# Performance work log

Measured on AMD Instinct MI355X. Metric: run time of the kernel, lower is better.

## Reference

```python
import jax, jax.numpy as jnp
import numpy as np

B, F, CHUNK = 4096, 1024, 128  # batch, features, scan chunk size
EPS = 1e-5  # nn.LayerNorm default eps


def setup_inputs() -> dict:
    key = jax.random.key(0)
    k1, k2 = jax.random.split(key, 2)
    x = jax.random.normal(k1, (B, F), dtype=jnp.float32)
    W = jax.random.normal(k2, (F, F), dtype=jnp.float32) * 0.5  # init_weight = randn*0.5
    b = jnp.zeros((F,), dtype=jnp.float32)
    gamma = jnp.ones((F,), dtype=jnp.float32)   # LayerNorm weight
    beta = jnp.zeros((F,), dtype=jnp.float32)   # LayerNorm bias
    return {"x": x, "W": W, "b": b, "gamma": gamma, "beta": beta}


def reference(x, W, b, gamma, beta):
    # LayerNorm over last dim (biased variance, as torch)
    mu = jnp.mean(x, axis=-1, keepdims=True)
    var = jnp.mean(jnp.square(x - mu), axis=-1, keepdims=True)
    xn = (x - mu) * jax.lax.rsqrt(var + EPS) * gamma + beta  # [B, F]

    # Tropical max-plus matmul: out[b, i] = max_k xn[b, k] + W[k, i]
    # Chunk the batch to avoid materializing the full [B, F, F] broadcast-add.
    xc = xn.reshape(B // CHUNK, CHUNK, F)

    def step(_, xb):  # xb: [CHUNK, F]
        o = jnp.max(xb[:, :, None] + W[None, :, :], axis=1)  # [CHUNK, F]
        return None, o

    _, out = jax.lax.scan(step, None, xc)
    out = out.reshape(B, F)

    # Tropical bias: elementwise max with learned threshold b
    return jnp.maximum(out, b)
```

## Files before the change

### kernel.cpp

```cpp
#include <hip/hip_runtime.h>
#include <math.h>

#define F 1024
#define BM 128
#define BN 128
#define BK 16

typedef _Float16 h2 __attribute__((ext_vector_type(2)));
typedef _Float16 h4 __attribute__((ext_vector_type(4)));
typedef _Float16 h8 __attribute__((ext_vector_type(8)));
typedef float v4f __attribute__((ext_vector_type(4)));

#define SHUF2(v, i, j) __builtin_shufflevector(v, v, i, j)
#define SHUF4(v, a, b, c, d) __builtin_shufflevector(v, v, a, b, c, d)

static __device__ __forceinline__ h2 pk_add_blo(h2 a, h2 b) {
  h2 d;
  asm("v_pk_add_f16 %0, %1, %2 op_sel:[0,0] op_sel_hi:[0,1]"
      : "=v"(d) : "v"(a), "v"(b));
  return d;
}
static __device__ __forceinline__ h2 pk_add_bhi(h2 a, h2 b) {
  h2 d;
  asm("v_pk_add_f16 %0, %1, %2 op_sel:[1,0] op_sel_hi:[1,1]"
      : "=v"(d) : "v"(a), "v"(b));
  return d;
}
static __device__ __forceinline__ h2 pk_max(h2 a, h2 b) {
  h2 d;
  asm("v_pk_max_f16 %0, %1, %2" : "=v"(d) : "v"(a), "v"(b));
  return d;
}

__global__ __launch_bounds__(256) void ln_cvt_kernel(const float* __restrict__ x,
                                                     const float* __restrict__ gamma,
                                                     const float* __restrict__ beta,
                                                     const float* __restrict__ Wm,
                                                     _Float16* __restrict__ xnh,
                                                     _Float16* __restrict__ Wh) {
  const int lane = threadIdx.x & 63;
  const int wv = threadIdx.x >> 6;
  const int row = blockIdx.x * 4 + wv;
  const float4* xr = (const float4*)(x + (size_t)row * F);
  float4 v[4];
  float s = 0.f;
#pragma unroll
  for (int j = 0; j < 4; ++j) {
    v[j] = xr[lane + 64 * j];
    s += v[j].x + v[j].y + v[j].z + v[j].w;
  }
#pragma unroll
  for (int off = 32; off; off >>= 1) s += __shfl_xor(s, off, 64);
  const float mu = s * (1.0f / F);
  float sq = 0.f;
#pragma unroll
  for (int j = 0; j < 4; ++j) {
    v[j].x -= mu; v[j].y -= mu; v[j].z -= mu; v[j].w -= mu;
    sq += v[j].x * v[j].x + v[j].y * v[j].y + v[j].z * v[j].z + v[j].w * v[j].w;
  }
#pragma unroll
  for (int off = 32; off; off >>= 1) sq += __shfl_xor(sq, off, 64);
  const float r = rsqrtf(sq * (1.0f / F) + 1e-5f);
  const float4* g4 = (const float4*)gamma;
  const float4* b4 = (const float4*)beta;
  h4* o = (h4*)(xnh + (size_t)row * F);
#pragma unroll
  for (int j = 0; j < 4; ++j) {
    const int idx = lane + 64 * j;
    const float4 g = g4[idx];
    const float4 bb = b4[idx];
    h4 ov = {(_Float16)(v[j].x * r * g.x + bb.x),
             (_Float16)(v[j].y * r * g.y + bb.y),
             (_Float16)(v[j].z * r * g.z + bb.z),
             (_Float16)(v[j].w * r * g.w + bb.w)};
    o[idx] = ov;
  }
  {
    const int i = (int)blockIdx.x * 256 + threadIdx.x;
    const v4f wv4 = ((const v4f*)Wm)[i];
    h4 wo = {(_Float16)wv4.x, (_Float16)wv4.y, (_Float16)wv4.z, (_Float16)wv4.w};
    ((h4*)Wh)[i] = wo;
  }
}

__global__ __launch_bounds__(256) void trop_h(const _Float16* __restrict__ A,
                                              const _Float16* __restrict__ Wh,
                                              const float* __restrict__ bias,
                                              _Float16* __restrict__ dsth,
                                              float* __restrict__ outf,
                                              int ntiles, int totrows, int fuse) {
  __shared__ _Float16 As[2][BM][BK + 4];
  __shared__ _Float16 Bs[2][BK][BN];

  const int tid = threadIdx.x;
  const int tx = tid & 15;
  const int ty = tid >> 4;
  const int row0 = blockIdx.y * BM;
  const int col0 = blockIdx.x * BN;
  const int kbase = blockIdx.z * ntiles * BK;

  const int am2 = tid >> 1, aj = tid & 1;
  const int bi = tid >> 4, bj = tid & 15;

  const _Float16* Asrc = A + (size_t)(row0 + am2) * F + kbase + aj * 8;
  const _Float16* Bsrc = Wh + (size_t)(kbase + bi) * F + col0 + bj * 8;

  const _Float16 NEG = (_Float16)(-60000.0f);
  h2 acc[8][4];
#pragma unroll
  for (int m = 0; m < 8; ++m)
#pragma unroll
    for (int np = 0; np < 4; ++np) acc[m][np] = (h2){NEG, NEG};

  {
    h8 a_st = *(const h8*)Asrc;
    h8 b_st = *(const h8*)Bsrc;
    *(h4*)&As[0][am2][aj * 8] = SHUF4(a_st, 0, 1, 2, 3);
    *(h4*)&As[0][am2][aj * 8 + 4] = SHUF4(a_st, 4, 5, 6, 7);
    *(h8*)&Bs[0][bi][bj * 8] = b_st;
  }
  __syncthreads();

  for (int kt = 0; kt < ntiles; ++kt) {
    const int cur = kt & 1;
    h8 a_st, b_st;
    if (kt + 1 < ntiles) {
      a_st = *(const h8*)(Asrc + (kt + 1) * BK);
      b_st = *(const h8*)(Bsrc + (size_t)(kt + 1) * BK * F);
    }

#pragma unroll
    for (int kq = 0; kq < 4; ++kq) {
      h4 a4[8];
#pragma unroll
      for (int m = 0; m < 8; ++m) a4[m] = *(const h4*)&As[cur][ty * 8 + m][kq * 4];
#pragma unroll
      for (int kp = 0; kp < 2; ++kp) {
        const int k = kq * 4 + kp * 2;
        const h8 bA = *(const h8*)&Bs[cur][k][tx * 8];
        const h8 bB = *(const h8*)&Bs[cur][k + 1][tx * 8];
        h2 b0[4], b1[4];
        b0[0] = SHUF2(bA, 0, 1); b0[1] = SHUF2(bA, 2, 3);
        b0[2] = SHUF2(bA, 4, 5); b0[3] = SHUF2(bA, 6, 7);
        b1[0] = SHUF2(bB, 0, 1); b1[1] = SHUF2(bB, 2, 3);
        b1[2] = SHUF2(bB, 4, 5); b1[3] = SHUF2(bB, 6, 7);
#pragma unroll
        for (int m = 0; m < 8; ++m) {
          const h2 a = kp ? SHUF2(a4[m], 2, 3) : SHUF2(a4[m], 0, 1);
#pragma unroll
          for (int np = 0; np < 4; ++np) {
            const h2 s0 = pk_add_blo(a, b0[np]);
            const h2 s1 = pk_add_bhi(a, b1[np]);
            acc[m][np] = pk_max(acc[m][np], pk_max(s0, s1));
          }
        }
      }
    }

    if (kt + 1 < ntiles) {
      const int nxt = cur ^ 1;
      *(h4*)&As[nxt][am2][aj * 8] = SHUF4(a_st, 0, 1, 2, 3);
      *(h4*)&As[nxt][am2][aj * 8 + 4] = SHUF4(a_st, 4, 5, 6, 7);
      *(h8*)&Bs[nxt][bi][bj * 8] = b_st;
      __syncthreads();
    }
  }

  if (fuse) {
    const float4 bv0 = *(const float4*)(bias + col0 + tx * 8);
    const float4 bv1 = *(const float4*)(bias + col0 + tx * 8 + 4);
#pragma unroll
    for (int m = 0; m < 8; ++m) {
      float* orow = outf + (size_t)(row0 + ty * 8 + m) * F + col0 + tx * 8;
      float4 o0, o1;
      o0.x = fmaxf((float)acc[m][0].x, bv0.x);
      o0.y = fmaxf((float)acc[m][0].y, bv0.y);
      o0.z = fmaxf((float)acc[m][1].x, bv0.z);
      o0.w = fmaxf((float)acc[m][1].y, bv0.w);
      o1.x = fmaxf((float)acc[m][2].x, bv1.x);
      o1.y = fmaxf((float)acc[m][2].y, bv1.y);
      o1.z = fmaxf((float)acc[m][3].x, bv1.z);
      o1.w = fmaxf((float)acc[m][3].y, bv1.w);
      *(float4*)orow = o0;
      *(float4*)(orow + 4) = o1;
    }
  } else {
    _Float16* base = dsth + (size_t)blockIdx.z * totrows * F;
#pragma unroll
    for (int m = 0; m < 8; ++m) {
      h8 ov = {acc[m][0].x, acc[m][0].y, acc[m][1].x, acc[m][1].y,
               acc[m][2].x, acc[m][2].y, acc[m][3].x, acc[m][3].y};
      *(h8*)(base + (size_t)(row0 + ty * 8 + m) * F + col0 + tx * 8) = ov;
    }
  }
}

template <int NP>
__global__ __launch_bounds__(256) void combineNh(const _Float16* __restrict__ p,
                                                 size_t plane,
                                                 const float* __restrict__ bias,
                                                 float* __restrict__ out) {
  const int i = blockIdx.x * 256 + threadIdx.x;
  h8 v = ((const h8*)p)[i];
  h2* vv = (h2*)&v;
#pragma unroll
  for (int q = 1; q < NP; ++q) {
    const h8 u = ((const h8*)(p + (size_t)q * plane))[i];
    const h2* uu = (const h2*)&u;
#pragma unroll
    for (int j = 0; j < 4; ++j) vv[j] = pk_max(vv[j], uu[j]);
  }
  const int nb = (i & (F / 8 - 1)) * 8;
  const v4f bb0 = *(const v4f*)(bias + nb);
  const v4f bb1 = *(const v4f*)(bias + nb + 4);
  float4* o4 = (float4*)(out + (size_t)i * 8);
  float4 o0, o1;
  o0.x = fmaxf((float)v[0], bb0.x);
  o0.y = fmaxf((float)v[1], bb0.y);
  o0.z = fmaxf((float)v[2], bb0.z);
  o0.w = fmaxf((float)v[3], bb0.w);
  o1.x = fmaxf((float)v[4], bb1.x);
  o1.y = fmaxf((float)v[5], bb1.y);
  o1.z = fmaxf((float)v[6], bb1.z);
  o1.w = fmaxf((float)v[7], bb1.w);
  o4[0] = o0;
  o4[1] = o1;
}

extern "C" void kernel_launch(void* const* d_in, const int* in_sizes, int n_in,
                              void* d_out, int out_size, void* d_ws, size_t ws_size,
                              hipStream_t stream) {
  const float* x = (const float*)d_in[0];
  const float* Wm = (const float*)d_in[1];
  const float* bias = (const float*)d_in[2];
  const float* gamma = (const float*)d_in[3];
  const float* beta = (const float*)d_in[4];
  float* out = (float*)d_out;

  const int Brows = in_sizes[0] / F;
  const size_t plane = (size_t)Brows * F;

  _Float16* xnh = (_Float16*)d_ws;
  _Float16* Wh = xnh + plane;
  _Float16* parts = Wh + (size_t)F * F;

  ln_cvt_kernel<<<Brows / 4, 256, 0, stream>>>(x, gamma, beta, Wm, xnh, Wh);

  const size_t need4 = (5 * plane + (size_t)F * F) * sizeof(_Float16);
  const size_t need1 = (plane + (size_t)F * F) * sizeof(_Float16);
  if (ws_size >= need4) {
    dim3 grid(F / BN, Brows / BM, 4);
    trop_h<<<grid, 256, 0, stream>>>(xnh, Wh, bias, parts, nullptr,
                                     (F / BK) / 4, Brows, 0);
    combineNh<4><<<(int)(plane / 2048), 256, 0, stream>>>(parts, plane, bias, out);
  } else if (ws_size >= need1) {
    dim3 grid(F / BN, Brows / BM, 1);
    trop_h<<<grid, 256, 0, stream>>>(xnh, Wh, bias, nullptr, out, F / BK, Brows, 1);
  }
}
```

Before: 220.1 us.

## Switch tropical matmul from packed fp16 to fp32 with max3

Replaces the packed-fp16 max-plus inner loop with an fp32 version using v_max3_f32 over two k-steps, reading W directly in fp32 and storing A transposed (K-major) in shared memory. The LayerNorm kernel now writes fp32 and no longer converts W to fp16. This improves numerical accuracy and removes a conversion pass, but doubles shared/global traffic per element and loses the 2-wide packed math throughput.

```diff
diff --git a/kernel.cpp b/kernel.cpp
--- a/kernel.cpp
+++ b/kernel.cpp
@@ -11,19 +11,9 @@
 typedef _Float16 h8 __attribute__((ext_vector_type(8)));
 typedef float v4f __attribute__((ext_vector_type(4)));
 
-#define SHUF2(v, i, j) __builtin_shufflevector(v, v, i, j)
-#define SHUF4(v, a, b, c, d) __builtin_shufflevector(v, v, a, b, c, d)
-
-static __device__ __forceinline__ h2 pk_add_blo(h2 a, h2 b) {
-  h2 d;
-  asm("v_pk_add_f16 %0, %1, %2 op_sel:[0,0] op_sel_hi:[0,1]"
-      : "=v"(d) : "v"(a), "v"(b));
-  return d;
-}
-static __device__ __forceinline__ h2 pk_add_bhi(h2 a, h2 b) {
-  h2 d;
-  asm("v_pk_add_f16 %0, %1, %2 op_sel:[1,0] op_sel_hi:[1,1]"
-      : "=v"(d) : "v"(a), "v"(b));
+static __device__ __forceinline__ float fmax3(float a, float b, float c) {
+  float d;
+  asm("v_max3_f32 %0, %1, %2, %3" : "=v"(d) : "v"(a), "v"(b), "v"(c));
   return d;
 }
 static __device__ __forceinline__ h2 pk_max(h2 a, h2 b) {
@@ -32,12 +22,10 @@
   return d;
 }
 
-__global__ __launch_bounds__(256) void ln_cvt_kernel(const float* __restrict__ x,
-                                                     const float* __restrict__ gamma,
-                                                     const float* __restrict__ beta,
-                                                     const float* __restrict__ Wm,
-                                                     _Float16* __restrict__ xnh,
-                                                     _Float16* __restrict__ Wh) {
+__global__ __launch_bounds__(256) void ln_kernel(const float* __restrict__ x,
+                                                 const float* __restrict__ gamma,
+                                                 const float* __restrict__ beta,
+                                                 float* __restrict__ xn) {
   const int lane = threadIdx.x & 63;
   const int wv = threadIdx.x >> 6;
   const int row = blockIdx.x * 4 + wv;
@@ -63,34 +51,29 @@
   const float r = rsqrtf(sq * (1.0f / F) + 1e-5f);
   const float4* g4 = (const float4*)gamma;
   const float4* b4 = (const float4*)beta;
-  h4* o = (h4*)(xnh + (size_t)row * F);
+  float4* o = (float4*)(xn + (size_t)row * F);
 #pragma unroll
   for (int j = 0; j < 4; ++j) {
     const int idx = lane + 64 * j;
     const float4 g = g4[idx];
     const float4 bb = b4[idx];
-    h4 ov = {(_Float16)(v[j].x * r * g.x + bb.x),
-             (_Float16)(v[j].y * r * g.y + bb.y),
-             (_Float16)(v[j].z * r * g.z + bb.z),
-             (_Float16)(v[j].w * r * g.w + bb.w)};
+    float4 ov;
+    ov.x = v[j].x * r * g.x + bb.x;
+    ov.y = v[j].y * r * g.y + bb.y;
+    ov.z = v[j].z * r * g.z + bb.z;
+    ov.w = v[j].w * r * g.w + bb.w;
     o[idx] = ov;
   }
-  {
-    const int i = (int)blockIdx.x * 256 + threadIdx.x;
-    const v4f wv4 = ((const v4f*)Wm)[i];
-    h4 wo = {(_Float16)wv4.x, (_Float16)wv4.y, (_Float16)wv4.z, (_Float16)wv4.w};
-    ((h4*)Wh)[i] = wo;
-  }
-}
-
-__global__ __launch_bounds__(256) void trop_h(const _Float16* __restrict__ A,
-                                              const _Float16* __restrict__ Wh,
-                                              const float* __restrict__ bias,
-                                              _Float16* __restrict__ dsth,
-                                              float* __restrict__ outf,
-                                              int ntiles, int totrows, int fuse) {
-  __shared__ _Float16 As[2][BM][BK + 4];
-  __shared__ _Float16 Bs[2][BK][BN];
+}
+
+__global__ __launch_bounds__(256, 4) void trop_f(const float* __restrict__ A,
+                                                 const float* __restrict__ Wm,
+                                                 const float* __restrict__ bias,
+                                                 _Float16* __restrict__ dsth,
+                                                 float* __restrict__ outf,
+                                                 int ntiles, int totrows, int fuse) {
+  __shared__ float As[2][BK][BM + 4];
+  __shared__ float Bs[2][BK][BN];
 
   const int tid = threadIdx.x;
   const int tx = tid & 15;
@@ -99,98 +82,119 @@
   const int col0 = blockIdx.x * BN;
   const int kbase = blockIdx.z * ntiles * BK;
 
-  const int am2 = tid >> 1, aj = tid & 1;
-  const int bi = tid >> 4, bj = tid & 15;
-
-  const _Float16* Asrc = A + (size_t)(row0 + am2) * F + kbase + aj * 8;
-  const _Float16* Bsrc = Wh + (size_t)(kbase + bi) * F + col0 + bj * 8;
-
-  const _Float16 NEG = (_Float16)(-60000.0f);
-  h2 acc[8][4];
+  const int am = tid >> 2;
+  const int ak = (tid & 3) << 2;
+  const int bk = tid >> 5;
+  const int bn = (tid & 31) << 2;
+
+  const float* Arow0 = A + (size_t)(row0 + am) * F + kbase + ak;
+  const float* Arow1 = A + (size_t)(row0 + am + 64) * F + kbase + ak;
+  const float* Wrow0 = Wm + (size_t)(kbase + bk) * F + col0 + bn;
+  const float* Wrow1 = Wm + (size_t)(kbase + bk + 8) * F + col0 + bn;
+
+  float acc[8][8];
 #pragma unroll
   for (int m = 0; m < 8; ++m)
 #pragma unroll
-    for (int np = 0; np < 4; ++np) acc[m][np] = (h2){NEG, NEG};
+    for (int n = 0; n < 8; ++n) acc[m][n] = -INFINITY;
 
   {
-    h8 a_st = *(const h8*)Asrc;
-    h8 b_st = *(const h8*)Bsrc;
-    *(h4*)&As[0][am2][aj * 8] = SHUF4(a_st, 0, 1, 2, 3);
-    *(h4*)&As[0][am2][aj * 8 + 4] = SHUF4(a_st, 4, 5, 6, 7);
-    *(h8*)&Bs[0][bi][bj * 8] = b_st;
+    const float4 a0s = *(const float4*)(Arow0);
+    const float4 a1s = *(const float4*)(Arow1);
+    const float4 b0s = *(const float4*)(Wrow0);
+    const float4 b1s = *(const float4*)(Wrow1);
+    As[0][ak + 0][am] = a0s.x;
+    As[0][ak + 1][am] = a0s.y;
+    As[0][ak + 2][am] = a0s.z;
+    As[0][ak + 3][am] = a0s.w;
+    As[0][ak + 0][am + 64] = a1s.x;
+    As[0][ak + 1][am + 64] = a1s.y;
+    As[0][ak + 2][am + 64] = a1s.z;
+    As[0][ak + 3][am + 64] = a1s.w;
+    *(float4*)&Bs[0][bk][bn] = b0s;
+    *(float4*)&Bs[0][bk + 8][bn] = b1s;
   }
   __syncthreads();
 
   for (int kt = 0; kt < ntiles; ++kt) {
     const int cur = kt & 1;
-    h8 a_st, b_st;
+    float4 a0s, a1s, b0s, b1s;
     if (kt + 1 < ntiles) {
-      a_st = *(const h8*)(Asrc + (kt + 1) * BK);
-      b_st = *(const h8*)(Bsrc + (size_t)(kt + 1) * BK * F);
-    }
-
-#pragma unroll
-    for (int kq = 0; kq < 4; ++kq) {
-      h4 a4[8];
-#pragma unroll
-      for (int m = 0; m < 8; ++m) a4[m] = *(const h4*)&As[cur][ty * 8 + m][kq * 4];
-#pragma unroll
-      for (int kp = 0; kp < 2; ++kp) {
-        const int k = kq * 4 + kp * 2;
-        const h8 bA = *(const h8*)&Bs[cur][k][tx * 8];
-        const h8 bB = *(const h8*)&Bs[cur][k + 1][tx * 8];
-        h2 b0[4], b1[4];
-        b0[0] = SHUF2(bA, 0, 1); b0[1] = SHUF2(bA, 2, 3);
-        b0[2] = SHUF2(bA, 4, 5); b0[3] = SHUF2(bA, 6, 7);
-        b1[0] = SHUF2(bB, 0, 1); b1[1] = SHUF2(bB, 2, 3);
-        b1[2] = SHUF2(bB, 4, 5); b1[3] = SHUF2(bB, 6, 7);
-#pragma unroll
-        for (int m = 0; m < 8; ++m) {
-          const h2 a = kp ? SHUF2(a4[m], 2, 3) : SHUF2(a4[m], 0, 1);
-#pragma unroll
-          for (int np = 0; np < 4; ++np) {
-            const h2 s0 = pk_add_blo(a, b0[np]);
-            const h2 s1 = pk_add_bhi(a, b1[np]);
-            acc[m][np] = pk_max(acc[m][np], pk_max(s0, s1));
+      const int k0 = (kt + 1) * BK;
+      a0s = *(const float4*)(Arow0 + k0);
+      a1s = *(const float4*)(Arow1 + k0);
+      b0s = *(const float4*)(Wrow0 + (size_t)k0 * F);
+      b1s = *(const float4*)(Wrow1 + (size_t)k0 * F);
+    }
+
+#pragma unroll
+    for (int k = 0; k < BK; k += 2) {
+      float a0[8], a1[8];
+      *(float4*)&a0[0] = *(const float4*)&As[cur][k][ty * 8];
+      *(float4*)&a0[4] = *(const float4*)&As[cur][k][ty * 8 + 4];
+      *(float4*)&a1[0] = *(const float4*)&As[cur][k + 1][ty * 8];
+      *(float4*)&a1[4] = *(const float4*)&As[cur][k + 1][ty * 8 + 4];
+#pragma unroll
+      for (int h = 0; h < 2; ++h) {
+        float b0[4], b1[4];
+        *(float4*)&b0[0] = *(const float4*)&Bs[cur][k][h * 64 + tx * 4];
+        *(float4*)&b1[0] = *(const float4*)&Bs[cur][k + 1][h * 64 + tx * 4];
+#pragma unroll
+        for (int m = 0; m < 8; ++m)
+#pragma unroll
+          for (int n = 0; n < 4; ++n) {
+            const float t0 = a0[m] + b0[n];
+            const float t1 = a1[m] + b1[n];
+            acc[m][h * 4 + n] = fmax3(acc[m][h * 4 + n], t0, t1);
           }
-        }
       }
     }
 
     if (kt + 1 < ntiles) {
       const int nxt = cur ^ 1;
-      *(h4*)&As[nxt][am2][aj * 8] = SHUF4(a_st, 0, 1, 2, 3);
-      *(h4*)&As[nxt][am2][aj * 8 + 4] = SHUF4(a_st, 4, 5, 6, 7);
-      *(h8*)&Bs[nxt][bi][bj * 8] = b_st;
+      As[nxt][ak + 0][am] = a0s.x;
+      As[nxt][ak + 1][am] = a0s.y;
+      As[nxt][ak + 2][am] = a0s.z;
+      As[nxt][ak + 3][am] = a0s.w;
+      As[nxt][ak + 0][am + 64] = a1s.x;
+      As[nxt][ak + 1][am + 64] = a1s.y;
+      As[nxt][ak + 2][am + 64] = a1s.z;
+      As[nxt][ak + 3][am + 64] = a1s.w;
+      *(float4*)&Bs[nxt][bk][bn] = b0s;
+      *(float4*)&Bs[nxt][bk + 8][bn] = b1s;
       __syncthreads();
     }
   }
 
   if (fuse) {
-    const float4 bv0 = *(const float4*)(bias + col0 + tx * 8);
-    const float4 bv1 = *(const float4*)(bias + col0 + tx * 8 + 4);
+    const float4 bv0 = *(const float4*)(bias + col0 + tx * 4);
+    const float4 bv1 = *(const float4*)(bias + col0 + 64 + tx * 4);
 #pragma unroll
     for (int m = 0; m < 8; ++m) {
-      float* orow = outf + (size_t)(row0 + ty * 8 + m) * F + col0 + tx * 8;
+      float* orow = outf + (size_t)(row0 + ty * 8 + m) * F + col0 + tx * 4;
       float4 o0, o1;
-      o0.x = fmaxf((float)acc[m][0].x, bv0.x);
-      o0.y = fmaxf((float)acc[m][0].y, bv0.y);
-      o0.z = fmaxf((float)acc[m][1].x, bv0.z);
-      o0.w = fmaxf((float)acc[m][1].y, bv0.w);
-      o1.x = fmaxf((float)acc[m][2].x, bv1.x);
-      o1.y = fmaxf((float)acc[m][2].y, bv1.y);
-      o1.z = fmaxf((float)acc[m][3].x, bv1.z);
-      o1.w = fmaxf((float)acc[m][3].y, bv1.w);
+      o0.x = fmaxf(acc[m][0], bv0.x);
+      o0.y = fmaxf(acc[m][1], bv0.y);
+      o0.z = fmaxf(acc[m][2], bv0.z);
+      o0.w = fmaxf(acc[m][3], bv0.w);
+      o1.x = fmaxf(acc[m][4], bv1.x);
+      o1.y = fmaxf(acc[m][5], bv1.y);
+      o1.z = fmaxf(acc[m][6], bv1.z);
+      o1.w = fmaxf(acc[m][7], bv1.w);
       *(float4*)orow = o0;
-      *(float4*)(orow + 4) = o1;
+      *(float4*)(orow + 64) = o1;
     }
   } else {
     _Float16* base = dsth + (size_t)blockIdx.z * totrows * F;
 #pragma unroll
     for (int m = 0; m < 8; ++m) {
-      h8 ov = {acc[m][0].x, acc[m][0].y, acc[m][1].x, acc[m][1].y,
-               acc[m][2].x, acc[m][2].y, acc[m][3].x, acc[m][3].y};
-      *(h8*)(base + (size_t)(row0 + ty * 8 + m) * F + col0 + tx * 8) = ov;
+      _Float16* orow = base + (size_t)(row0 + ty * 8 + m) * F + col0 + tx * 4;
+      h4 o0 = {(_Float16)acc[m][0], (_Float16)acc[m][1],
+               (_Float16)acc[m][2], (_Float16)acc[m][3]};
+      h4 o1 = {(_Float16)acc[m][4], (_Float16)acc[m][5],
+               (_Float16)acc[m][6], (_Float16)acc[m][7]};
+      *(h4*)orow = o0;
+      *(h4*)(orow + 64) = o1;
     }
   }
 }
@@ -240,21 +244,20 @@
   const int Brows = in_sizes[0] / F;
   const size_t plane = (size_t)Brows * F;
 
-  _Float16* xnh = (_Float16*)d_ws;
-  _Float16* Wh = xnh + plane;
-  _Float16* parts = Wh + (size_t)F * F;
-
-  ln_cvt_kernel<<<Brows / 4, 256, 0, stream>>>(x, gamma, beta, Wm, xnh, Wh);
-
-  const size_t need4 = (5 * plane + (size_t)F * F) * sizeof(_Float16);
-  const size_t need1 = (plane + (size_t)F * F) * sizeof(_Float16);
+  float* xn = (float*)d_ws;
+  _Float16* parts = (_Float16*)(xn + plane);
+
+  ln_kernel<<<Brows / 4, 256, 0, stream>>>(x, gamma, beta, xn);
+
+  const size_t need4 = plane * sizeof(float) + 4 * plane * sizeof(_Float16);
+  const size_t need1 = plane * sizeof(float);
   if (ws_size >= need4) {
     dim3 grid(F / BN, Brows / BM, 4);
-    trop_h<<<grid, 256, 0, stream>>>(xnh, Wh, bias, parts, nullptr,
+    trop_f<<<grid, 256, 0, stream>>>(xn, Wm, bias, parts, nullptr,
                                      (F / BK) / 4, Brows, 0);
     combineNh<4><<<(int)(plane / 2048), 256, 0, stream>>>(parts, plane, bias, out);
   } else if (ws_size >= need1) {
     dim3 grid(F / BN, Brows / BM, 1);
-    trop_h<<<grid, 256, 0, stream>>>(xnh, Wh, bias, nullptr, out, F / BK, Brows, 1);
-  }
-}
+    trop_f<<<grid, 256, 0, stream>>>(xn, Wm, bias, nullptr, out, F / BK, Brows, 1);
+  }
+}
```

New measurement: 210.3 us. 1.05x faster.

## Accumulate max-plus in fp32 via fma_mix and max3 with transposed A tile

Applied to the files above, without the earlier changes.

Replaces the packed fp16 add/max inner loop with v_fma_mix_f32, which adds fp16 inputs into fp32 results, and v_max3_f32, which folds two k-steps per max. Accumulators become fp32 (64 floats per thread). The A tile is stored k-major in shared memory so rows can be read as vectors, and the B column mapping becomes interleaved (tx*4 and 64+tx*4) to change the LDS access pattern. This gives more accurate accumulation. The cost is roughly twice as many VALU ops per output, since the packed fp16 ops did two elements each, plus higher register pressure under a 4-waves launch bound.

```diff
diff --git a/kernel.cpp b/kernel.cpp
--- a/kernel.cpp
+++ b/kernel.cpp
@@ -12,18 +12,34 @@
 typedef float v4f __attribute__((ext_vector_type(4)));
 
 #define SHUF2(v, i, j) __builtin_shufflevector(v, v, i, j)
-#define SHUF4(v, a, b, c, d) __builtin_shufflevector(v, v, a, b, c, d)
-
-static __device__ __forceinline__ h2 pk_add_blo(h2 a, h2 b) {
-  h2 d;
-  asm("v_pk_add_f16 %0, %1, %2 op_sel:[0,0] op_sel_hi:[0,1]"
-      : "=v"(d) : "v"(a), "v"(b));
-  return d;
-}
-static __device__ __forceinline__ h2 pk_add_bhi(h2 a, h2 b) {
-  h2 d;
-  asm("v_pk_add_f16 %0, %1, %2 op_sel:[1,0] op_sel_hi:[1,1]"
-      : "=v"(d) : "v"(a), "v"(b));
+
+static __device__ __forceinline__ float mix_ll(h2 a, h2 b) {
+  float d;
+  asm("v_fma_mix_f32 %0, %1, 1.0, %2 op_sel:[0,0,0] op_sel_hi:[1,0,1]"
+      : "=v"(d) : "v"(a), "v"(b));
+  return d;
+}
+static __device__ __forceinline__ float mix_lh(h2 a, h2 b) {
+  float d;
+  asm("v_fma_mix_f32 %0, %1, 1.0, %2 op_sel:[0,0,1] op_sel_hi:[1,0,1]"
+      : "=v"(d) : "v"(a), "v"(b));
+  return d;
+}
+static __device__ __forceinline__ float mix_hl(h2 a, h2 b) {
+  float d;
+  asm("v_fma_mix_f32 %0, %1, 1.0, %2 op_sel:[1,0,0] op_sel_hi:[1,0,1]"
+      : "=v"(d) : "v"(a), "v"(b));
+  return d;
+}
+static __device__ __forceinline__ float mix_hh(h2 a, h2 b) {
+  float d;
+  asm("v_fma_mix_f32 %0, %1, 1.0, %2 op_sel:[1,0,1] op_sel_hi:[1,0,1]"
+      : "=v"(d) : "v"(a), "v"(b));
+  return d;
+}
+static __device__ __forceinline__ float fmax3(float a, float b, float c) {
+  float d;
+  asm("v_max3_f32 %0, %1, %2, %3" : "=v"(d) : "v"(a), "v"(b), "v"(c));
   return d;
 }
 static __device__ __forceinline__ h2 pk_max(h2 a, h2 b) {
@@ -83,13 +99,13 @@
   }
 }
 
-__global__ __launch_bounds__(256) void trop_h(const _Float16* __restrict__ A,
-                                              const _Float16* __restrict__ Wh,
-                                              const float* __restrict__ bias,
-                                              _Float16* __restrict__ dsth,
-                                              float* __restrict__ outf,
-                                              int ntiles, int totrows, int fuse) {
-  __shared__ _Float16 As[2][BM][BK + 4];
+__global__ __launch_bounds__(256, 4) void trop_m(const _Float16* __restrict__ A,
+                                                 const _Float16* __restrict__ Wh,
+                                                 const float* __restrict__ bias,
+                                                 _Float16* __restrict__ dsth,
+                                                 float* __restrict__ outf,
+                                                 int ntiles, int totrows, int fuse) {
+  __shared__ _Float16 As[2][BK][BM + 8];
   __shared__ _Float16 Bs[2][BK][BN];
 
   const int tid = threadIdx.x;
@@ -99,25 +115,26 @@
   const int col0 = blockIdx.x * BN;
   const int kbase = blockIdx.z * ntiles * BK;
 
-  const int am2 = tid >> 1, aj = tid & 1;
-  const int bi = tid >> 4, bj = tid & 15;
-
-  const _Float16* Asrc = A + (size_t)(row0 + am2) * F + kbase + aj * 8;
-  const _Float16* Bsrc = Wh + (size_t)(kbase + bi) * F + col0 + bj * 8;
-
-  const _Float16 NEG = (_Float16)(-60000.0f);
-  h2 acc[8][4];
+  const int ar = tid >> 1;
+  const int akj = (tid & 1) * 8;
+  const int bkr = tid >> 4;
+  const int bcg = (tid & 15) * 8;
+
+  const _Float16* Asrc = A + (size_t)(row0 + ar) * F + kbase + akj;
+  const _Float16* Bsrc = Wh + (size_t)(kbase + bkr) * F + col0 + bcg;
+
+  float acc[8][8];
 #pragma unroll
   for (int m = 0; m < 8; ++m)
 #pragma unroll
-    for (int np = 0; np < 4; ++np) acc[m][np] = (h2){NEG, NEG};
+    for (int n = 0; n < 8; ++n) acc[m][n] = -INFINITY;
 
   {
-    h8 a_st = *(const h8*)Asrc;
-    h8 b_st = *(const h8*)Bsrc;
-    *(h4*)&As[0][am2][aj * 8] = SHUF4(a_st, 0, 1, 2, 3);
-    *(h4*)&As[0][am2][aj * 8 + 4] = SHUF4(a_st, 4, 5, 6, 7);
-    *(h8*)&Bs[0][bi][bj * 8] = b_st;
+    const h8 a_st = *(const h8*)Asrc;
+    const h8 b_st = *(const h8*)Bsrc;
+#pragma unroll
+    for (int j = 0; j < 8; ++j) As[0][akj + j][ar] = a_st[j];
+    *(h8*)&Bs[0][bkr][bcg] = b_st;
   }
   __syncthreads();
 
@@ -130,67 +147,79 @@
     }
 
 #pragma unroll
-    for (int kq = 0; kq < 4; ++kq) {
-      h4 a4[8];
-#pragma unroll
-      for (int m = 0; m < 8; ++m) a4[m] = *(const h4*)&As[cur][ty * 8 + m][kq * 4];
-#pragma unroll
-      for (int kp = 0; kp < 2; ++kp) {
-        const int k = kq * 4 + kp * 2;
-        const h8 bA = *(const h8*)&Bs[cur][k][tx * 8];
-        const h8 bB = *(const h8*)&Bs[cur][k + 1][tx * 8];
-        h2 b0[4], b1[4];
-        b0[0] = SHUF2(bA, 0, 1); b0[1] = SHUF2(bA, 2, 3);
-        b0[2] = SHUF2(bA, 4, 5); b0[3] = SHUF2(bA, 6, 7);
-        b1[0] = SHUF2(bB, 0, 1); b1[1] = SHUF2(bB, 2, 3);
-        b1[2] = SHUF2(bB, 4, 5); b1[3] = SHUF2(bB, 6, 7);
-#pragma unroll
-        for (int m = 0; m < 8; ++m) {
-          const h2 a = kp ? SHUF2(a4[m], 2, 3) : SHUF2(a4[m], 0, 1);
-#pragma unroll
-          for (int np = 0; np < 4; ++np) {
-            const h2 s0 = pk_add_blo(a, b0[np]);
-            const h2 s1 = pk_add_bhi(a, b1[np]);
-            acc[m][np] = pk_max(acc[m][np], pk_max(s0, s1));
-          }
+    for (int k = 0; k < BK; k += 2) {
+      union { h8 v; h2 p[4]; } a0u, a1u;
+      a0u.v = *(const h8*)&As[cur][k][ty * 8];
+      a1u.v = *(const h8*)&As[cur][k + 1][ty * 8];
+      const h4 b0a = *(const h4*)&Bs[cur][k][tx * 4];
+      const h4 b0b = *(const h4*)&Bs[cur][k][64 + tx * 4];
+      const h4 b1a = *(const h4*)&Bs[cur][k + 1][tx * 4];
+      const h4 b1b = *(const h4*)&Bs[cur][k + 1][64 + tx * 4];
+      h2 b0[4], b1[4];
+      b0[0] = SHUF2(b0a, 0, 1); b0[1] = SHUF2(b0a, 2, 3);
+      b0[2] = SHUF2(b0b, 0, 1); b0[3] = SHUF2(b0b, 2, 3);
+      b1[0] = SHUF2(b1a, 0, 1); b1[1] = SHUF2(b1a, 2, 3);
+      b1[2] = SHUF2(b1b, 0, 1); b1[3] = SHUF2(b1b, 2, 3);
+#pragma unroll
+      for (int mp = 0; mp < 4; ++mp) {
+        const h2 a0p = a0u.p[mp];
+        const h2 a1p = a1u.p[mp];
+#pragma unroll
+        for (int q = 0; q < 4; ++q) {
+          const float t00 = mix_ll(a0p, b0[q]);
+          const float t01 = mix_lh(a0p, b0[q]);
+          const float t10 = mix_ll(a1p, b1[q]);
+          const float t11 = mix_lh(a1p, b1[q]);
+          acc[2 * mp][2 * q]     = fmax3(acc[2 * mp][2 * q], t00, t10);
+          acc[2 * mp][2 * q + 1] = fmax3(acc[2 * mp][2 * q + 1], t01, t11);
+          const float u00 = mix_hl(a0p, b0[q]);
+          const float u01 = mix_hh(a0p, b0[q]);
+          const float u10 = mix_hl(a1p, b1[q]);
+          const float u11 = mix_hh(a1p, b1[q]);
+          acc[2 * mp + 1][2 * q]     = fmax3(acc[2 * mp + 1][2 * q], u00, u10);
+          acc[2 * mp + 1][2 * q + 1] = fmax3(acc[2 * mp + 1][2 * q + 1], u01, u11);
         }
       }
     }
 
     if (kt + 1 < ntiles) {
       const int nxt = cur ^ 1;
-      *(h4*)&As[nxt][am2][aj * 8] = SHUF4(a_st, 0, 1, 2, 3);
-      *(h4*)&As[nxt][am2][aj * 8 + 4] = SHUF4(a_st, 4, 5, 6, 7);
-      *(h8*)&Bs[nxt][bi][bj * 8] = b_st;
+#pragma unroll
+      for (int j = 0; j < 8; ++j) As[nxt][akj + j][ar] = a_st[j];
+      *(h8*)&Bs[nxt][bkr][bcg] = b_st;
       __syncthreads();
     }
   }
 
   if (fuse) {
-    const float4 bv0 = *(const float4*)(bias + col0 + tx * 8);
-    const float4 bv1 = *(const float4*)(bias + col0 + tx * 8 + 4);
+    const float4 bv0 = *(const float4*)(bias + col0 + tx * 4);
+    const float4 bv1 = *(const float4*)(bias + col0 + 64 + tx * 4);
 #pragma unroll
     for (int m = 0; m < 8; ++m) {
-      float* orow = outf + (size_t)(row0 + ty * 8 + m) * F + col0 + tx * 8;
+      float* orow = outf + (size_t)(row0 + ty * 8 + m) * F + col0 + tx * 4;
       float4 o0, o1;
-      o0.x = fmaxf((float)acc[m][0].x, bv0.x);
-      o0.y = fmaxf((float)acc[m][0].y, bv0.y);
-      o0.z = fmaxf((float)acc[m][1].x, bv0.z);
-      o0.w = fmaxf((float)acc[m][1].y, bv0.w);
-      o1.x = fmaxf((float)acc[m][2].x, bv1.x);
-      o1.y = fmaxf((float)acc[m][2].y, bv1.y);
-      o1.z = fmaxf((float)acc[m][3].x, bv1.z);
-      o1.w = fmaxf((float)acc[m][3].y, bv1.w);
+      o0.x = fmaxf(acc[m][0], bv0.x);
+      o0.y = fmaxf(acc[m][1], bv0.y);
+      o0.z = fmaxf(acc[m][2], bv0.z);
+      o0.w = fmaxf(acc[m][3], bv0.w);
+      o1.x = fmaxf(acc[m][4], bv1.x);
+      o1.y = fmaxf(acc[m][5], bv1.y);
+      o1.z = fmaxf(acc[m][6], bv1.z);
+      o1.w = fmaxf(acc[m][7], bv1.w);
       *(float4*)orow = o0;
-      *(float4*)(orow + 4) = o1;
+      *(float4*)(orow + 64) = o1;
     }
   } else {
     _Float16* base = dsth + (size_t)blockIdx.z * totrows * F;
 #pragma unroll
     for (int m = 0; m < 8; ++m) {
-      h8 ov = {acc[m][0].x, acc[m][0].y, acc[m][1].x, acc[m][1].y,
-               acc[m][2].x, acc[m][2].y, acc[m][3].x, acc[m][3].y};
-      *(h8*)(base + (size_t)(row0 + ty * 8 + m) * F + col0 + tx * 8) = ov;
+      _Float16* orow = base + (size_t)(row0 + ty * 8 + m) * F + col0 + tx * 4;
+      h4 o0 = {(_Float16)acc[m][0], (_Float16)acc[m][1],
+               (_Float16)acc[m][2], (_Float16)acc[m][3]};
+      h4 o1 = {(_Float16)acc[m][4], (_Float16)acc[m][5],
+               (_Float16)acc[m][6], (_Float16)acc[m][7]};
+      *(h4*)orow = o0;
+      *(h4*)(orow + 64) = o1;
     }
   }
 }
@@ -250,11 +279,11 @@
   const size_t need1 = (plane + (size_t)F * F) * sizeof(_Float16);
   if (ws_size >= need4) {
     dim3 grid(F / BN, Brows / BM, 4);
-    trop_h<<<grid, 256, 0, stream>>>(xnh, Wh, bias, parts, nullptr,
+    trop_m<<<grid, 256, 0, stream>>>(xnh, Wh, bias, parts, nullptr,
                                      (F / BK) / 4, Brows, 0);
     combineNh<4><<<(int)(plane / 2048), 256, 0, stream>>>(parts, plane, bias, out);
   } else if (ws_size >= need1) {
     dim3 grid(F / BN, Brows / BM, 1);
-    trop_h<<<grid, 256, 0, stream>>>(xnh, Wh, bias, nullptr, out, F / BK, Brows, 1);
-  }
-}
+    trop_m<<<grid, 256, 0, stream>>>(xnh, Wh, bias, nullptr, out, F / BK, Brows, 1);
+  }
+}
```

After: 266.3 us. 21.0% more time.
